# Performance work log

Measured on AMD Instinct MI355X. Metric: run time of the kernel, lower is better.

## Reference

```python
import jax, jax.numpy as jnp
import numpy as np

N_NODES = 50000
N_EDGES = 800000
D = 64
N_LAYERS = 5
N_GRAPHS = 256
N_CLASSES = 10
BN_EPS = 1e-5


def setup_inputs() -> dict:
    key = jax.random.key(0)
    ks = jax.random.split(key, 16)
    s = 1.0 / np.sqrt(D)
    return {
        "X": jax.random.normal(ks[0], (N_NODES, D), jnp.float32),
        "edge_index": jax.random.randint(ks[1], (2, N_EDGES), 0, N_NODES, jnp.int64),
        "batch": jnp.sort(jax.random.randint(ks[2], (N_NODES,), 0, N_GRAPHS, jnp.int64)),
        "Wk": jax.random.normal(ks[3], (N_LAYERS, D, D), jnp.float32) * s,
        "Wq": jax.random.normal(ks[4], (N_LAYERS, D, D), jnp.float32) * s,
        "Wv": jax.random.normal(ks[5], (N_LAYERS, D, D), jnp.float32) * s,
        "Ws": jax.random.normal(ks[6], (N_LAYERS, D, D), jnp.float32) * s,
        "bk": jnp.zeros((N_LAYERS, D), jnp.float32),
        "bq": jnp.zeros((N_LAYERS, D), jnp.float32),
        "bv": jnp.zeros((N_LAYERS, D), jnp.float32),
        "bconv": jnp.zeros((N_LAYERS, D), jnp.float32),
        "gamma": jnp.ones((N_LAYERS, D), jnp.float32),
        "beta": jnp.zeros((N_LAYERS, D), jnp.float32),
        "Wlin": jax.random.normal(ks[7], (D, N_CLASSES), jnp.float32) * s,
        "blin": jnp.zeros((N_CLASSES,), jnp.float32),
    }


def _res_gated_conv(x, src, dst, Wk, Wq, Wv, Ws, bk, bq, bv, b):
    # PyG ResGatedGraphConv: out_i = W_skip x_i + b + sum_{j->i} sigmoid(K x_i + Q x_j) * (V x_j)
    k = x @ Wk + bk  # [N, D]
    q = x @ Wq + bq
    v = x @ Wv + bv
    eta = jax.nn.sigmoid(k[dst] + q[src])         # [E, D] gate
    agg = jax.ops.segment_sum(eta * v[src], dst, num_segments=x.shape[0])
    return agg + x @ Ws + b


def _batch_norm(x, gamma, beta):
    mean = jnp.mean(x, axis=0)
    var = jnp.mean(jnp.square(x - mean), axis=0)  # biased, as torch BN training
    return (x - mean) * jax.lax.rsqrt(var + BN_EPS) * gamma + beta


def reference(X, edge_index, batch, Wk, Wq, Wv, Ws, bk, bq, bv, bconv, gamma, beta, Wlin, blin):
    src, dst = edge_index[0], edge_index[1]
    h = X
    for l in range(N_LAYERS):  # dropout_prob = 0 -> dropout is identity
        h = _res_gated_conv(h, src, dst, Wk[l], Wq[l], Wv[l], Ws[l], bk[l], bq[l], bv[l], bconv[l])
        h = jax.nn.relu(h)
        h = _batch_norm(h, gamma[l], beta[l])
    # global mean pool over graphs
    sums = jax.ops.segment_sum(h, batch, num_segments=N_GRAPHS)
    counts = jax.ops.segment_sum(jnp.ones((h.shape[0], 1), h.dtype), batch, num_segments=N_GRAPHS)
    pooled = sums / jnp.maximum(counts, 1.0)
    logits = pooled @ Wlin + blin
    return jax.nn.softmax(logits, axis=-1)
```

## Files before the change

kernel.cpp:

```cpp
#include <hip/hip_runtime.h>

#define NN 50000
#define NE 800000
#define DD 64
#define NL 5
#define NG 256
#define NC 10
#define BN_EPS 1e-5f
#define NCHUNK ((NN + 255) / 256)
#define GROWS 128
#define GT (GROWS / 16)
#define SAW 68
#define GEMM_BLOCKS ((NN + GROWS - 1) / GROWS)
#define NNS (NN + 8)
#define PADDEG(d) (((d) + 7) & ~7)
#define DEG_BLOCKS ((NE + 255) / 256)
#define WPREP_BLOCKS ((NL * 2048 + 255) / 256)
#define FCHK 2048
#define FCHUNKS ((NE + FCHK - 1) / FCHK)
#define FILLP_BLOCKS (8 * FCHUNKS)
#define NRANGE (NN / 8)
#define PAD_BLOCKS NCHUNK
#define L2E 1.4426950408889634f

typedef __attribute__((ext_vector_type(8))) short bf16x8;
typedef __attribute__((ext_vector_type(4))) float f32x4;

__device__ inline float bf2f(unsigned short u) {
    return __uint_as_float((unsigned)u << 16);
}
__device__ inline unsigned short f2bf(float x) {
    unsigned u = __float_as_uint(x);
    u += 0x7FFFu + ((u >> 16) & 1u);
    return (unsigned short)(u >> 16);
}

__device__ inline unsigned int pack_bf16x2(float a, float b) {
    unsigned int ua = __float_as_uint(a);
    unsigned int ub = __float_as_uint(b);
    ua += 0x7FFFu + ((ua >> 16) & 1u);
    ub += 0x7FFFu + ((ub >> 16) & 1u);
    return (ub & 0xFFFF0000u) | (ua >> 16);
}

__device__ inline void split_bf16(float x, short& h, short& l) {
    const unsigned u  = __float_as_uint(x);
    const unsigned hb = u & 0xFFFF0000u;
    h = (short)(hb >> 16);
    const float lo = x - __uint_as_float(hb);
    l = (short)(__float_as_uint(lo) >> 16);
}

__device__ inline float p_eq(unsigned p) { return __uint_as_float(p << 16); }
__device__ inline float p_v(unsigned p)  { return __uint_as_float(p & 0xFFFF0000u); }

#define GPAIR(ek, pa, pb, acc) { \
    const float t1_ = fmaf(ek, p_eq(pa), 1.f); \
    const float t2_ = fmaf(ek, p_eq(pb), 1.f); \
    const float R_  = __builtin_amdgcn_rcpf(t1_ * t2_); \
    acc = fmaf(fmaf(p_v(pb), t1_, p_v(pa) * t2_), R_, acc); }

#define GCOLS(ekx, eky, p, accx, accy) { \
    const float t1_ = fmaf(ekx, p_eq(p.x), 1.f); \
    const float t2_ = fmaf(eky, p_eq(p.y), 1.f); \
    const float R_  = __builtin_amdgcn_rcpf(t1_ * t2_); \
    accx = fmaf(p_v(p.x), R_ * t2_, accx); \
    accy = fmaf(p_v(p.y), R_ * t1_, accy); }

template<int F32>
__device__ __forceinline__ void gemm_body(
    const void* __restrict__ HinV,
    const bf16x8* __restrict__ whbuf, const bf16x8* __restrict__ wlbuf,
    const float* __restrict__ bk, const float* __restrict__ bq,
    const float* __restrict__ bv, const float* __restrict__ bs,
    const float* __restrict__ prevStats,
    const float* __restrict__ prevGamma, const float* __restrict__ prevBeta,
    unsigned short* __restrict__ Kq, unsigned int* __restrict__ QVq,
    unsigned short* __restrict__ Hq, const int gb)
{
    __shared__ unsigned int sA[GROWS * SAW];
    __shared__ float sAB[128];
    const int tid = threadIdx.x;

    if (!F32) {
        if (tid < 64) {
            const float invN = 1.0f / (float)NN;
            const float mean = prevStats[tid] * invN;
            const float var  = prevStats[64 + tid] * invN - mean * mean;
            const float inv  = rsqrtf(var + BN_EPS);
            const float a = inv * prevGamma[tid];
            sAB[tid]      = a;
            sAB[64 + tid] = prevBeta[tid] - mean * a;
        }
        __syncthreads();
    }

    const int row0 = gb * GROWS;
    if (F32) {
        const float* X = (const float*)HinV;
        for (int i = tid; i < GROWS * 16; i += 256) {
            const int row = i >> 4;
            const int k4  = (i & 15) * 4;
            float4 x = make_float4(0.f, 0.f, 0.f, 0.f);
            if (row0 + row < NN)
                x = *(const float4*)(X + (size_t)(row0 + row) * DD + k4);
            const float xs[4] = {x.x, x.y, x.z, x.w};
            unsigned int* dst = &sA[row * SAW + k4];
#pragma unroll
            for (int j = 0; j < 4; j++) {
                short hs, ls;
                split_bf16(xs[j], hs, ls);
                dst[j] = ((unsigned int)(unsigned short)hs << 16) | (unsigned short)ls;
            }
        }
    } else {
        const unsigned short* Hin = (const unsigned short*)HinV;
        for (int i = tid; i < GROWS * 8; i += 256) {
            const int row = i >> 3;
            const int cb  = (i & 7) * 8;
            const int q   = cb >> 4;
            const int o16 = cb & 15;
            uint4 v = make_uint4(0u, 0u, 0u, 0u);
            if (row0 + row < NN)
                v = *(const uint4*)&Hin[((size_t)q * NN + row0 + row) * 16 + o16];
            const unsigned ws[4] = {v.x, v.y, v.z, v.w};
            unsigned int* dst = &sA[row * SAW + cb];
#pragma unroll
            for (int j = 0; j < 4; j++) {
                const float x0 = bf2f((unsigned short)(ws[j] & 0xFFFFu));
                const float x1 = bf2f((unsigned short)(ws[j] >> 16));
                const int c0 = cb + 2 * j, c1 = cb + 2 * j + 1;
                short hs, ls;
                split_bf16(fmaf(x0, sAB[c0], sAB[64 + c0]), hs, ls);
                dst[2 * j] = ((unsigned int)(unsigned short)hs << 16) | (unsigned short)ls;
                split_bf16(fmaf(x1, sAB[c1], sAB[64 + c1]), hs, ls);
                dst[2 * j + 1] = ((unsigned int)(unsigned short)hs << 16) | (unsigned short)ls;
            }
        }
    }

    const int wave = tid >> 6;
    const int lane = tid & 63;
    const int n15  = lane & 15;
    const int g    = lane >> 4;
    const int col  = wave * 16 + n15;

    bf16x8 wh[4][2], wl[4][2];
    {
        const int base = wave * 64 + lane;
#pragma unroll
        for (int m = 0; m < 4; m++)
#pragma unroll
            for (int c = 0; c < 2; c++) {
                const int idx = m * 512 + c * 256 + base;
                wh[m][c] = whbuf[idx];
                wl[m][c] = wlbuf[idx];
            }
    }

    const float nbk = -bk[col] * L2E;
    const float nbq = -bq[col] * L2E;
    const float bvc = bv[col], bsc = bs[col];
    __syncthreads();

#pragma unroll 1
    for (int t = 0; t < GT; t++) {
        const int rowbase = row0 + t * 16;
        if (rowbase >= NN) break;

        bf16x8 ah[2], al[2];
#pragma unroll
        for (int c = 0; c < 2; c++) {
            const uint4 u0 = *(const uint4*)&sA[(t * 16 + n15) * SAW + g * 8 + 32 * c];
            const uint4 u1 = *(const uint4*)&sA[(t * 16 + n15) * SAW + g * 8 + 32 * c + 4];
            const unsigned int us[8] = {u0.x, u0.y, u0.z, u0.w, u1.x, u1.y, u1.z, u1.w};
            bf16x8 h, l;
#pragma unroll
            for (int j = 0; j < 8; j++) {
                h[j] = (short)(us[j] >> 16);
                l[j] = (short)(us[j] & 0xFFFFu);
            }
            ah[c] = h; al[c] = l;
        }

        f32x4 acc[4];
#pragma unroll
        for (int m = 0; m < 4; m++) acc[m] = (f32x4){0.f, 0.f, 0.f, 0.f};

#pragma unroll
        for (int c = 0; c < 2; c++) {
#pragma unroll
            for (int m = 0; m < 4; m++) {
                acc[m] = __builtin_amdgcn_mfma_f32_16x16x32_bf16(ah[c], wh[m][c], acc[m], 0, 0, 0);
                acc[m] = __builtin_amdgcn_mfma_f32_16x16x32_bf16(al[c], wh[m][c], acc[m], 0, 0, 0);
                acc[m] = __builtin_amdgcn_mfma_f32_16x16x32_bf16(ah[c], wl[m][c], acc[m], 0, 0, 0);
            }
        }

#pragma unroll
        for (int r = 0; r < 4; r++) {
            const int row = rowbase + g * 4 + r;
            const size_t o  = ((size_t)wave * NN  + row) * 16 + n15;
            const size_t oq = ((size_t)wave * NNS + row) * 16 + n15;
            Kq[o]   = f2bf(__builtin_amdgcn_exp2f(fmaf(acc[0][r], -L2E, nbk)));
            QVq[oq] = pack_bf16x2(__builtin_amdgcn_exp2f(fmaf(acc[1][r], -L2E, nbq)),
                                  acc[2][r] + bvc);
            Hq[o]   = f2bf(acc[3][r] + bsc);
        }
    }
}

__global__ __launch_bounds__(256) void prep_kernel(
    const int* __restrict__ ei, int* __restrict__ deg,
    const float* __restrict__ Wk, const float* __restrict__ Wq,
    const float* __restrict__ Wv, const float* __restrict__ Ws,
    bf16x8* __restrict__ whbuf, bf16x8* __restrict__ wlbuf,
    unsigned int* __restrict__ QVq)
{
    const int bid = blockIdx.x;
    if (bid < DEG_BLOCKS) {
        const int e = bid * 256 + threadIdx.x;
        if (e < NE) atomicAdd(&deg[ei[NE + e]], 1);
        return;
    }
    if (bid == DEG_BLOCKS && threadIdx.x < 64) {
        const int q = threadIdx.x >> 4, c = threadIdx.x & 15;
        QVq[((size_t)q * NNS + NN) * 16 + c] = 0u;
    }
    const int t = (bid - DEG_BLOCKS) * 256 + threadIdx.x;
    if (t >= NL * 2048) return;
    const int lane = t & 63;
    const int w    = (t >> 6) & 3;
    const int c    = (t >> 8) & 1;
    const int m    = (t >> 9) & 3;
    const int l    = t >> 11;

    const float* Wm4[4] = {Wk, Wq, Wv, Ws};
    const float* W = Wm4[m] + l * 4096;
    const int col = w * 16 + (lane & 15);
    const int g   = lane >> 4;

    bf16x8 h, lo;
#pragma unroll
    for (int j = 0; j < 8; j++) {
        const int k = g * 8 + j + 32 * c;
        short hs, ls;
        split_bf16(W[k * DD + col], hs, ls);
        h[j] = hs; lo[j] = ls;
    }
    whbuf[t] = h;
    wlbuf[t] = lo;
}

__global__ __launch_bounds__(256) void scan_partial_kernel(
    const int* __restrict__ deg, int* __restrict__ psums)
{
    __shared__ int ls[256];
    const int i = blockIdx.x * 256 + threadIdx.x;
    ls[threadIdx.x] = (i < NN) ? PADDEG(deg[i]) : 0;
    __syncthreads();
    for (int off = 128; off > 0; off >>= 1) {
        if (threadIdx.x < off) ls[threadIdx.x] += ls[threadIdx.x + off];
        __syncthreads();
    }
    if (threadIdx.x == 0) psums[blockIdx.x] = ls[0];
}

__global__ void scan_offsets_kernel(int* __restrict__ psums, int* __restrict__ rowst)
{
    if (threadIdx.x == 0) {
        int running = 0;
        for (int i = 0; i < NCHUNK; i++) {
            int t = psums[i];
            psums[i] = running;
            running += t;
        }
        rowst[NN] = running;
    }
}

__global__ __launch_bounds__(256) void scan_final_kernel(
    const int* __restrict__ deg, const int* __restrict__ psums,
    int* __restrict__ rowst, int* __restrict__ cursor)
{
    __shared__ int ls[256];
    const int i = blockIdx.x * 256 + threadIdx.x;
    const int x = (i < NN) ? PADDEG(deg[i]) : 0;
    ls[threadIdx.x] = x;
    __syncthreads();
    for (int off = 1; off < 256; off <<= 1) {
        int v = (threadIdx.x >= off) ? ls[threadIdx.x - off] : 0;
        __syncthreads();
        ls[threadIdx.x] += v;
        __syncthreads();
    }
    if (i < NN) {
        const int excl = psums[blockIdx.x] + ls[threadIdx.x] - x;
        rowst[i]  = excl;
        cursor[i] = excl;
    }
}

__global__ __launch_bounds__(256) void gfp_kernel(
    const float* __restrict__ X,
    const bf16x8* __restrict__ whbuf, const bf16x8* __restrict__ wlbuf,
    const float* __restrict__ bk, const float* __restrict__ bq,
    const float* __restrict__ bv, const float* __restrict__ bs,
    unsigned short* __restrict__ Kq, unsigned int* __restrict__ QVq,
    unsigned short* __restrict__ Hq,
    const int* __restrict__ ei, int* __restrict__ cursor,
    const int* __restrict__ rowst, const int* __restrict__ deg,
    unsigned short* __restrict__ csr16)
{
    const int bid = blockIdx.x;
    if (bid < GEMM_BLOCKS) {
        gemm_body<1>(X, whbuf, wlbuf, bk, bq, bv, bs,
                     nullptr, nullptr, nullptr, Kq, QVq, Hq, bid);
        return;
    }
    if (bid < GEMM_BLOCKS + FILLP_BLOCKS) {
        const int fid = bid - GEMM_BLOCKS;
        const int r   = bid & 7;
        const int o   = fid >> 3;
        const int lo  = r * NRANGE;
        const int hi  = lo + NRANGE;
        const int e0  = o * FCHK;
        const int e1  = min(e0 + FCHK, NE);
        for (int e = e0 + threadIdx.x; e < e1; e += 256) {
            const int dst = ei[NE + e];
            if (dst >= lo && dst < hi) {
                const int src = ei[e];
                csr16[atomicAdd(&cursor[dst], 1)] = (unsigned short)src;
            }
        }
        return;
    }
    const int n = (bid - GEMM_BLOCKS - FILLP_BLOCKS) * 256 + threadIdx.x;
    if (n >= NN) return;
    const int end = rowst[n + 1];
    for (int i = rowst[n] + deg[n]; i < end; i++) csr16[i] = (unsigned short)NN;
}

__global__ __launch_bounds__(256) void gemm4_mfma(
    const void* __restrict__ HinV,
    const bf16x8* __restrict__ whbuf, const bf16x8* __restrict__ wlbuf,
    const float* __restrict__ bk, const float* __restrict__ bq,
    const float* __restrict__ bv, const float* __restrict__ bs,
    const float* __restrict__ prevStats,
    const float* __restrict__ prevGamma, const float* __restrict__ prevBeta,
    unsigned short* __restrict__ Kq, unsigned int* __restrict__ QVq,
    unsigned short* __restrict__ Hq)
{
    gemm_body<0>(HinV, whbuf, wlbuf, bk, bq, bv, bs,
                 prevStats, prevGamma, prevBeta, Kq, QVq, Hq, blockIdx.x);
}

#define GATHER_BLOCKS (8 * 782)
__global__ __launch_bounds__(256) void gather_kernel(
    const int* __restrict__ rowst, const unsigned short* __restrict__ csr16,
    const unsigned short* __restrict__ Kq, const unsigned int* __restrict__ QVq,
    unsigned short* Hq, float* __restrict__ stats)
{
    const int tid  = threadIdx.x;
    const int wv   = tid >> 6;
    const int lane = tid & 63;
    const int eoff = lane >> 3;
    const int cp   = lane & 7;

    const int j       = blockIdx.x;
    const int xcd     = j & 7;
    const int quarter = xcd >> 1;
    const int half    = xcd & 1;
    const int nodebase = ((j >> 3) * 2 + half) * 32 + wv * 8;

    const unsigned* Kq32 = (const unsigned*)(Kq + (size_t)quarter * NN * 16);
    const uint2*    Qq2  = (const uint2*)(QVq + (size_t)quarter * NNS * 16);
    unsigned*       Hq32 = (unsigned*)(Hq + (size_t)quarter * NN * 16);

    float se = 0.f, s2e = 0.f, so = 0.f, s2o = 0.f;

    int e00 = rowst[min(nodebase, NN)];

    for (int t = 0; t < 4; t++) {
        const int n0 = nodebase + 2 * t;
        if (n0 >= NN) break;
        const int n1 = n0 + 1;
        const unsigned ho0 = (unsigned)(n0 * 8 + cp);
        const unsigned ho1 = (unsigned)(n1 * 8 + cp);
        unsigned h0p = 0u, h1p = 0u;
        if (eoff == 0) {
            h0p = Hq32[ho0];
            h1p = Hq32[ho1];
        }
        const unsigned k0p = Kq32[ho0];
        const unsigned k1p = Kq32[ho1];
        const float ek00 = bf2f((unsigned short)(k0p & 0xFFFFu));
        const float ek01 = bf2f((unsigned short)(k0p >> 16));
        const float ek10 = bf2f((unsigned short)(k1p & 0xFFFFu));
        const float ek11 = bf2f((unsigned short)(k1p >> 16));
        const int e01 = rowst[n1], e11 = rowst[n1 + 1];
        int nd0 = (e01 - e00) >> 3;
        int nd1 = (e11 - e01) >> 3;
        int ndm = min(nd0, nd1);
        nd0 -= ndm; nd1 -= ndm;
        int b0 = e00, b1 = e01;
        e00 = e11;
        float a00 = 0.f, a01 = 0.f, a10 = 0.f, a11 = 0.f;

        while (ndm >= 2) {
            const unsigned s0 = *(const unsigned*)(csr16 + b0 + 2 * eoff);
            const unsigned s1 = *(const unsigned*)(csr16 + b1 + 2 * eoff);
            const uint2 p0a = Qq2[(s0 & 0xFFFFu) * 8u + cp];
            const uint2 p0b = Qq2[(s0 >> 16) * 8u + cp];
            const uint2 p1a = Qq2[(s1 & 0xFFFFu) * 8u + cp];
            const uint2 p1b = Qq2[(s1 >> 16) * 8u + cp];
            GPAIR(ek00, p0a.x, p0b.x, a00);
            GPAIR(ek01, p0a.y, p0b.y, a01);
            GPAIR(ek10, p1a.x, p1b.x, a10);
            GPAIR(ek11, p1a.y, p1b.y, a11);
            b0 += 16; b1 += 16; ndm -= 2;
        }
        if (ndm) {
            const int s0 = csr16[b0 + eoff];
            const int s1 = csr16[b1 + eoff];
            const uint2 p0 = Qq2[(unsigned)(s0 * 8 + cp)];
            const uint2 p1 = Qq2[(unsigned)(s1 * 8 + cp)];
            GCOLS(ek00, ek01, p0, a00, a01);
            GCOLS(ek10, ek11, p1, a10, a11);
            b0 += 8; b1 += 8;
        }
        while (nd0 >= 2) {
            const unsigned s0 = *(const unsigned*)(csr16 + b0 + 2 * eoff);
            const uint2 p0a = Qq2[(s0 & 0xFFFFu) * 8u + cp];
            const uint2 p0b = Qq2[(s0 >> 16) * 8u + cp];
            GPAIR(ek00, p0a.x, p0b.x, a00);
            GPAIR(ek01, p0a.y, p0b.y, a01);
            b0 += 16; nd0 -= 2;
        }
        if (nd0) {
            const int s0 = csr16[b0 + eoff];
            const uint2 p0 = Qq2[(unsigned)(s0 * 8 + cp)];
            GCOLS(ek00, ek01, p0, a00, a01);
        }
        while (nd1 >= 2) {
            const unsigned s1 = *(const unsigned*)(csr16 + b1 + 2 * eoff);
            const uint2 p1a = Qq2[(s1 & 0xFFFFu) * 8u + cp];
            const uint2 p1b = Qq2[(s1 >> 16) * 8u + cp];
            GPAIR(ek10, p1a.x, p1b.x, a10);
            GPAIR(ek11, p1a.y, p1b.y, a11);
            b1 += 16; nd1 -= 2;
        }
        if (nd1) {
            const int s1 = csr16[b1 + eoff];
            const uint2 p1 = Qq2[(unsigned)(s1 * 8 + cp)];
            GCOLS(ek10, ek11, p1, a10, a11);
        }

        a00 += __shfl_xor(a00, 8);  a00 += __shfl_xor(a00, 16); a00 += __shfl_xor(a00, 32);
        a01 += __shfl_xor(a01, 8);  a01 += __shfl_xor(a01, 16); a01 += __shfl_xor(a01, 32);
        a10 += __shfl_xor(a10, 8);  a10 += __shfl_xor(a10, 16); a10 += __shfl_xor(a10, 32);
        a11 += __shfl_xor(a11, 8);  a11 += __shfl_xor(a11, 16); a11 += __shfl_xor(a11, 32);

        if (eoff == 0) {
            const float o00 = fmaxf(bf2f((unsigned short)(h0p & 0xFFFFu)) + a00, 0.f);
            const float o01 = fmaxf(bf2f((unsigned short)(h0p >> 16))     + a01, 0.f);
            const float o10 = fmaxf(bf2f((unsigned short)(h1p & 0xFFFFu)) + a10, 0.f);
            const float o11 = fmaxf(bf2f((unsigned short)(h1p >> 16))     + a11, 0.f);
            const unsigned short b00 = f2bf(o00), b01 = f2bf(o01);
            const unsigned short b10 = f2bf(o10), b11 = f2bf(o11);
            Hq32[ho0] = ((unsigned)b01 << 16) | b00;
            Hq32[ho1] = ((unsigned)b11 << 16) | b10;
            const float r00 = bf2f(b00), r01 = bf2f(b01);
            const float r10 = bf2f(b10), r11 = bf2f(b11);
            se  += r00 + r10;  s2e += r00 * r00 + r10 * r10;
            so  += r01 + r11;  s2o += r01 * r01 + r11 * r11;
        }
    }

    __shared__ float ls[64], ls2[64];
    if (eoff == 0) {
        ls[wv * 16 + 2 * cp]      = se;  ls2[wv * 16 + 2 * cp]      = s2e;
        ls[wv * 16 + 2 * cp + 1]  = so;  ls2[wv * 16 + 2 * cp + 1]  = s2o;
    }
    __syncthreads();
    if (tid < 16) {
        const float a = ls[tid] + ls[16 + tid] + ls[32 + tid] + ls[48 + tid];
        const float b = ls2[tid] + ls2[16 + tid] + ls2[32 + tid] + ls2[48 + tid];
        atomicAdd(&stats[quarter * 16 + tid], a);
        atomicAdd(&stats[64 + quarter * 16 + tid], b);
    }
}

#define POOL_ROWS 64
__global__ __launch_bounds__(256) void pool_kernel(
    const unsigned short* __restrict__ Hq, const int* __restrict__ batch,
    float* __restrict__ psum, float* __restrict__ pcnt)
{
    const int sub = threadIdx.x >> 5;
    const int c   = threadIdx.x & 31;
    const int q   = c >> 3;
    const int p   = c & 7;
    const int r0 = (blockIdx.x * 8 + sub) * POOL_ROWS;
    if (r0 >= NN) return;
    const int r1 = min(r0 + POOL_ROWS, NN);
    const unsigned* Hqq = (const unsigned*)(Hq + (size_t)q * NN * 16);
    const int col0 = q * 16 + 2 * p;

    int cur = batch[r0];
    float acc0 = 0.f, acc1 = 0.f, cnt = 0.f;
    for (int r = r0; r < r1; r++) {
        const int g = batch[r];
        if (g != cur) {
            atomicAdd(&psum[cur * DD + col0], acc0);
            atomicAdd(&psum[cur * DD + col0 + 1], acc1);
            if (c == 0) atomicAdd(&pcnt[cur], cnt);
            acc0 = 0.f; acc1 = 0.f; cnt = 0.f; cur = g;
        }
        const unsigned hv = Hqq[(size_t)r * 8 + p];
        acc0 += bf2f((unsigned short)(hv & 0xFFFFu));
        acc1 += bf2f((unsigned short)(hv >> 16));
        cnt += 1.f;
    }
    atomicAdd(&psum[cur * DD + col0], acc0);
    atomicAdd(&psum[cur * DD + col0 + 1], acc1);
    if (c == 0) atomicAdd(&pcnt[cur], cnt);
}

__global__ __launch_bounds__(256) void final_kernel(
    const float* __restrict__ psum, const float* __restrict__ pcnt,
    const float* __restrict__ stats,
    const float* __restrict__ gamma, const float* __restrict__ beta,
    const float* __restrict__ Wlin, const float* __restrict__ blin,
    float* __restrict__ out)
{
    const int g = blockIdx.x * blockDim.x + threadIdx.x;
    if (g >= NG) return;

    const float invc = 1.0f / fmaxf(pcnt[g], 1.0f);
    const float invN = 1.0f / (float)NN;
    float p[DD];
#pragma unroll
    for (int d = 0; d < DD; d++) {
        const float mean = stats[d] * invN;
        const float var  = stats[64 + d] * invN - mean * mean;
        const float inv  = rsqrtf(var + BN_EPS);
        const float a = inv * gamma[d];
        const float b = beta[d] - mean * a;
        p[d] = fmaf(psum[g * DD + d] * invc, a, b);
    }

    float logits[NC];
    float m = -1e30f;
#pragma unroll
    for (int c = 0; c < NC; c++) {
        float acc = blin[c];
#pragma unroll
        for (int d = 0; d < DD; d++) acc = fmaf(p[d], Wlin[d * NC + c], acc);
        logits[c] = acc;
        m = fmaxf(m, acc);
    }
    float sum = 0.f;
#pragma unroll
    for (int c = 0; c < NC; c++) {
        logits[c] = __expf(logits[c] - m);
        sum += logits[c];
    }
    const float inv = 1.f / sum;
#pragma unroll
    for (int c = 0; c < NC; c++) out[g * NC + c] = logits[c] * inv;
}

extern "C" void kernel_launch(void* const* d_in, const int* in_sizes, int n_in,
                              void* d_out, int out_size, void* d_ws, size_t ws_size,
                              hipStream_t stream)
{
    const float* X     = (const float*)d_in[0];
    const int*   ei    = (const int*)d_in[1];
    const int*   batch = (const int*)d_in[2];
    const float* Wk    = (const float*)d_in[3];
    const float* Wq    = (const float*)d_in[4];
    const float* Wv    = (const float*)d_in[5];
    const float* Ws    = (const float*)d_in[6];
    const float* bk    = (const float*)d_in[7];
    const float* bq    = (const float*)d_in[8];
    const float* bv    = (const float*)d_in[9];
    const float* bconv = (const float*)d_in[10];
    const float* gamma = (const float*)d_in[11];
    const float* beta  = (const float*)d_in[12];
    const float* Wlin  = (const float*)d_in[13];
    const float* blin  = (const float*)d_in[14];
    float* out = (float*)d_out;

    const size_t M  = (size_t)NN * DD;
    const size_t MQ = (size_t)4 * NNS * 16;
    unsigned short* Kq  = (unsigned short*)d_ws;
    unsigned int*   QVq = (unsigned int*)(Kq + M);
    unsigned short* H0q = (unsigned short*)(QVq + MQ);
    unsigned short* H1q = H0q + M;
    int*   deg   = (int*)(H1q + M);
    float* psum  = (float*)(deg + NN);
    float* pcnt  = psum + (size_t)NG * DD;
    float* stats = pcnt + NG;
    int* rowst  = (int*)(stats + NL * 128);
    int* cursor = rowst + NN + 1;
    int* psums  = cursor + NN;
    unsigned short* csr16 = (unsigned short*)(psums + 256);
    bf16x8* whbuf = (bf16x8*)(csr16 + NE + 8 * NN);
    bf16x8* wlbuf = whbuf + NL * 2048;

    const size_t zero_bytes = (size_t)(NN + NG * DD + NG + NL * 128) * sizeof(float);
    hipMemsetAsync(deg, 0, zero_bytes, stream);

    prep_kernel<<<DEG_BLOCKS + WPREP_BLOCKS, 256, 0, stream>>>(
        ei, deg, Wk, Wq, Wv, Ws, whbuf, wlbuf, QVq);

    scan_partial_kernel<<<NCHUNK, 256, 0, stream>>>(deg, psums);
    scan_offsets_kernel<<<1, 64, 0, stream>>>(psums, rowst);
    scan_final_kernel<<<NCHUNK, 256, 0, stream>>>(deg, psums, rowst, cursor);

    gfp_kernel<<<GEMM_BLOCKS + FILLP_BLOCKS + PAD_BLOCKS, 256, 0, stream>>>(
        X, whbuf, wlbuf, bk, bq, bv, bconv,
        Kq, QVq, H0q, ei, cursor, rowst, deg, csr16);

    gather_kernel<<<GATHER_BLOCKS, 256, 0, stream>>>(
        rowst, csr16, Kq, QVq, H0q, stats);
    const void* hin = (const void*)H0q;
    for (int l = 1; l < NL; l++) {
        unsigned short* hout = (l & 1) ? H1q : H0q;
        gemm4_mfma<<<GEMM_BLOCKS, 256, 0, stream>>>(
            hin, whbuf + l * 2048, wlbuf + l * 2048,
            bk + l * 64, bq + l * 64, bv + l * 64, bconv + l * 64,
            stats + (l - 1) * 128, gamma + (l - 1) * 64, beta + (l - 1) * 64,
            Kq, QVq, hout);
        gather_kernel<<<GATHER_BLOCKS, 256, 0, stream>>>(
            rowst, csr16, Kq, QVq, hout, stats + l * 128);
        hin = (const void*)hout;
    }

    pool_kernel<<<(NN + 8 * POOL_ROWS - 1) / (8 * POOL_ROWS), 256, 0, stream>>>(
        (const unsigned short*)hin, batch, psum, pcnt);
    final_kernel<<<1, 256, 0, stream>>>(
        psum, pcnt, stats + 4 * 128, gamma + 4 * 64, beta + 4 * 64, Wlin, blin, out);
}
```

Measured before the change: 529.1 us.

## Halve GEMM tile rows, wave-parallel offset scan, uniform rowst loads

```diff
diff --git a/kernel.cpp b/kernel.cpp
--- a/kernel.cpp
+++ b/kernel.cpp
@@ -8,7 +8,7 @@
 #define NC 10
 #define BN_EPS 1e-5f
 #define NCHUNK ((NN + 255) / 256)
-#define GROWS 128
+#define GROWS 64
 #define GT (GROWS / 16)
 #define SAW 68
 #define GEMM_BLOCKS ((NN + GROWS - 1) / GROWS)
@@ -266,17 +266,31 @@
     if (threadIdx.x == 0) psums[blockIdx.x] = ls[0];
 }
 
-__global__ void scan_offsets_kernel(int* __restrict__ psums, int* __restrict__ rowst)
-{
-    if (threadIdx.x == 0) {
-        int running = 0;
-        for (int i = 0; i < NCHUNK; i++) {
-            int t = psums[i];
-            psums[i] = running;
-            running += t;
-        }
-        rowst[NN] = running;
-    }
+__global__ __launch_bounds__(64) void scan_offsets_kernel(
+    int* __restrict__ psums, int* __restrict__ rowst)
+{
+    const int lane = threadIdx.x;
+    const int base = lane * 4;
+    int v[4];
+    int s = 0;
+#pragma unroll
+    for (int j = 0; j < 4; j++) {
+        v[j] = (base + j < NCHUNK) ? psums[base + j] : 0;
+        s += v[j];
+    }
+    int incl = s;
+    for (int off = 1; off < 64; off <<= 1) {
+        const int t = __shfl_up(incl, off);
+        if (lane >= off) incl += t;
+    }
+    const int total = __shfl(incl, 63);
+    int run = incl - s;
+#pragma unroll
+    for (int j = 0; j < 4; j++) {
+        if (base + j < NCHUNK) psums[base + j] = run;
+        run += v[j];
+    }
+    if (lane == 0) rowst[NN] = total;
 }
 
 __global__ __launch_bounds__(256) void scan_final_kernel(
@@ -379,7 +393,7 @@
 
     float se = 0.f, s2e = 0.f, so = 0.f, s2o = 0.f;
 
-    int e00 = rowst[min(nodebase, NN)];
+    int e00 = __builtin_amdgcn_readfirstlane(rowst[min(nodebase, NN)]);
 
     for (int t = 0; t < 4; t++) {
         const int n0 = nodebase + 2 * t;
@@ -398,7 +412,8 @@
         const float ek01 = bf2f((unsigned short)(k0p >> 16));
         const float ek10 = bf2f((unsigned short)(k1p & 0xFFFFu));
         const float ek11 = bf2f((unsigned short)(k1p >> 16));
-        const int e01 = rowst[n1], e11 = rowst[n1 + 1];
+        const int e01 = __builtin_amdgcn_readfirstlane(rowst[n1]);
+        const int e11 = __builtin_amdgcn_readfirstlane(rowst[n1 + 1]);
         int nd0 = (e01 - e00) >> 3;
         int nd1 = (e11 - e01) >> 3;
         int ndm = min(nd0, nd1);
```

Result: no change. 533.8 us (+0.9%).
